# Performance work log

Hardware: AMD Instinct MI355X
Metric: run time of the kernel (lower is better)

Reference implementation:

```python
import jax, jax.numpy as jnp
import numpy as np

NODE_FEAT = 200  # F.interpolate size in run_all_node
TOPN = 2         # StitchModel.topn


def _node_feats(img, mask, flow, n_inst, max_pix):
    """Vectorized run_all_node: per-instance gather, linear interp to NODE_FEAT,
    3x3 sign histogram of flow[:2], mean of flow[2]. mask holds labels 1..n_inst;
    max_pix is a static upper bound on pixels per instance."""
    flat = mask.reshape(-1) - 1                       # labels 0..N-1
    order = jnp.argsort(flat)                         # stable sort by label
    counts = jax.ops.segment_sum(jnp.ones_like(flat), flat, num_segments=n_inst)
    starts = jnp.concatenate([jnp.zeros((1,), counts.dtype), jnp.cumsum(counts)[:-1]])
    j = jnp.arange(max_pix)
    pos = starts[:, None] + jnp.minimum(j[None, :], counts[:, None] - 1)
    idx = order[pos]                                  # [N, max_pix] padded pixel indices
    valid = j[None, :] < counts[:, None]              # [N, max_pix]
    iv = img.reshape(-1)[idx]                         # instance intensity profiles
    fx = flow[0].reshape(-1)[idx]
    fy = flow[1].reshape(-1)[idx]
    fz = flow[2].reshape(-1)[idx]
    cf = counts.astype(img.dtype)
    zflow = jnp.where(valid, fz, 0).sum(1) / cf       # flows[-1][m].mean()

    def interp(v, L):                                 # torch linear interp, align_corners=False
        Lf = L.astype(img.dtype)
        p = jnp.clip((jnp.arange(NODE_FEAT, dtype=img.dtype) + 0.5) * (Lf / NODE_FEAT) - 0.5,
                     0.0, Lf - 1.0)
        i0 = jnp.floor(p).astype(jnp.int32)
        i1 = jnp.minimum(i0 + 1, L - 1)
        w = p - i0.astype(img.dtype)
        return v[i0] * (1 - w) + v[i1] * w

    nodes = jax.vmap(interp)(iv, counts)              # [N, 200]
    # hist_flow_vector: bins ordered (x:<0,==0,>0) x (y:<0,==0,>0) -> 3*cx+cy
    cx = jnp.where(fx < 0, 0, jnp.where(fx == 0, 1, 2))
    cy = jnp.where(fy < 0, 0, jnp.where(fy == 0, 1, 2))
    bins = cx * 3 + cy
    oh = (bins[..., None] == jnp.arange(9)) & valid[..., None]
    hist = oh.sum(1).astype(img.dtype)                # [N, 9]
    return jnp.concatenate([nodes, hist], -1), zflow


def setup_inputs() -> dict:
    H = W = 2048
    N = 4096
    pix = (H * W) // N
    key = jax.random.key(0)
    ks = jax.random.split(key, 8)

    def make_mask(k):
        labels = (jnp.arange(H * W, dtype=jnp.int32) // pix) + 1   # labels 1..N
        perm = jax.random.permutation(k, H * W)
        return labels[perm].reshape(H, W)

    def make_bbox(k):
        u = jax.random.uniform(k, (N, 4), jnp.float32)
        centers = u[:, :2] * H
        sizes = u[:, 2:] * 49.0 + 1.0                               # nonzero w/h (asserted)
        return jnp.concatenate([centers, sizes], -1)

    return {
        "img1": jax.random.normal(ks[0], (H, W), jnp.float32),
        "img2": jax.random.normal(ks[1], (H, W), jnp.float32),
        "flow1": jax.random.normal(ks[2], (3, H, W), jnp.float32),
        "flow2": jax.random.normal(ks[3], (3, H, W), jnp.float32),
        "bbox1": make_bbox(ks[4]),
        "bbox2": make_bbox(ks[5]),
        "mask1": make_mask(ks[6]),
        "mask2": make_mask(ks[7]),
    }


def reference(img1, img2, flow1, flow2, bbox1, bbox2, mask1, mask2):
    N1, N2 = bbox1.shape[0], bbox2.shape[0]
    max1 = mask1.size // N1   # static bound on pixels/instance (equal-partition masks)
    max2 = mask2.size // N2
    node1, zf1 = _node_feats(img1, mask1, flow1, N1, max1)
    node2, zf2 = _node_feats(img2, mask2, flow2, N2, max2)
    x = jnp.concatenate([node1, node2], 0)            # [(N1+N2), 209]
    # build_one_graph_low_ram: per row, TOPN smallest center distances
    d = jnp.sqrt(((bbox1[:, None, :2] - bbox2[None, :, :2]) ** 2).sum(-1))  # [N1,N2]
    _, nbr = jax.lax.top_k(-d, TOPN)                  # smallest-first, like argsort[:topn]
    src = jnp.repeat(jnp.arange(N1), TOPN)            # [N1*TOPN]
    dst = nbr.reshape(-1)
    edge_index = jnp.stack([src, dst + N1])           # [2, N1*TOPN]
    edge_attr = jnp.stack([
        zf1[src], zf2[dst],
        bbox1[src, 0] - bbox2[dst, 0],
        bbox1[src, 1] - bbox2[dst, 1],
        bbox1[src, 2] / bbox2[dst, 2],
        bbox1[src, 3] / bbox2[dst, 3],
    ], -1)                                            # [N1*TOPN, 6]
    return x, edge_index, edge_attr
```

## Files before the change

kernel.cpp:

```cpp
#include <hip/hip_runtime.h>
#include <math.h>

#pragma clang fp contract(off)

#define HW      (2048*2048)
#define NI      4096
#define MAXPIX  1024
#define NF      200
#define FEAT    209
#define NE      (NI*2)
#define XSIZE   ((2*NI)*FEAT)
#define EIOFF   XSIZE
#define EAOFF   (EIOFF + 2*NE)

#define S       8192
#define CHK     (HW/S)
#define TOTCHK  (2*CHK)
#define NBPI    256
#define LPB     16
#define NBG     (2*NBPI)
#define REC     (2*HW)
#define CBLK    (TOTCHK/4)
#define BTOT    (LPB*MAXPIX)

template<int NB>
__device__ __forceinline__ unsigned long long match_bits(int v) {
    unsigned long long m = ~0ull;
    #pragma unroll
    for (int bit = 0; bit < NB; ++bit) {
        unsigned long long bb = __ballot((v >> bit) & 1);
        m &= ((v >> bit) & 1) ? bb : ~bb;
    }
    return m;
}

__global__ void __launch_bounds__(256) count_zf_kernel(const int* __restrict__ mask1,
        const int* __restrict__ mask2, const float* __restrict__ flow1,
        const float* __restrict__ flow2, unsigned* __restrict__ cntA,
        float* __restrict__ zfpart) {
    __shared__ unsigned cnt[4][NBPI];
    __shared__ float zfp[NI];
    int w = threadIdx.x >> 6, lane = threadIdx.x & 63;
    for (int j = threadIdx.x; j < 4*NBPI; j += 256) ((unsigned*)cnt)[j] = 0u;
    for (int j = threadIdx.x; j < NI; j += 256) zfp[j] = 0.f;
    __syncthreads();
    int c = blockIdx.x * 4 + w;
    int img = c / CHK;
    const int4*   mask  = (const int4*)(img ? mask2 : mask1);
    const float4* flowz = (const float4*)((img ? flow2 : flow1) + 2L*HW);
    long base4 = (long)(c - img*CHK) * (S/4);
    for (int t = 0; t < S/4; t += 64) {
        int4   l4 = mask[base4 + t + lane];
        float4 fz = flowz[base4 + t + lane];
        atomicAdd(&cnt[w][(l4.x-1) >> 4], 1u);
        atomicAdd(&cnt[w][(l4.y-1) >> 4], 1u);
        atomicAdd(&cnt[w][(l4.z-1) >> 4], 1u);
        atomicAdd(&cnt[w][(l4.w-1) >> 4], 1u);
        atomicAdd(&zfp[l4.x-1], fz.x);
        atomicAdd(&zfp[l4.y-1], fz.y);
        atomicAdd(&zfp[l4.z-1], fz.z);
        atomicAdd(&zfp[l4.w-1], fz.w);
    }
    __syncthreads();
    unsigned* dst = cntA + (long)c * NBPI;
    for (int j = lane; j < NBPI; j += 64) dst[j] = cnt[w][j];
    float* zdst = zfpart + (long)blockIdx.x * NI;
    for (int j = threadIdx.x; j < NI; j += 256) zdst[j] = zfp[j];
}

__global__ void __launch_bounds__(256) scan1_zf_kernel(unsigned* __restrict__ cntA,
        const float* __restrict__ zfpart, float* __restrict__ zfm) {
    __shared__ int wsum[4];
    __shared__ float zpar[16][LPB];
    int gb = blockIdx.x;
    int img = gb >> 8, lb = gb & (NBPI - 1);
    int t = threadIdx.x, lane = t & 63, w = t >> 6;
    const int PER = CHK / 256;
    unsigned e[PER]; int s = 0;
    long base = ((long)img * CHK + (long)t * PER) * NBPI + lb;
    #pragma unroll
    for (int i = 0; i < PER; ++i) { e[i] = cntA[base + (long)i * NBPI]; s += (int)e[i]; }
    int incl = s;
    #pragma unroll
    for (int off = 1; off < 64; off <<= 1) {
        int o = __shfl_up(incl, off);
        if (lane >= off) incl += o;
    }
    if (lane == 63) wsum[w] = incl;
    __syncthreads();
    int add = 0;
    for (int q = 0; q < w; ++q) add += wsum[q];
    unsigned pre = (unsigned)(incl + add - s);
    #pragma unroll
    for (int i = 0; i < PER; ++i) { unsigned cv = e[i]; cntA[base + (long)i * NBPI] = pre; pre += cv; }
    {
        int li0 = gb * LPB;
        int zimg = li0 >> 12, l0 = li0 & (NI-1);
        int lab = t & 15, rg = t >> 4;
        const float* zp = zfpart + (long)(zimg*(CBLK/2) + rg*8)*NI + l0 + lab;
        float s8 = 0.f;
        #pragma unroll
        for (int k = 0; k < 8; ++k) s8 += zp[(long)k*NI];
        zpar[rg][lab] = s8;
    }
    __syncthreads();
    if (t < LPB) {
        float sum = 0.f;
        #pragma unroll
        for (int g = 0; g < 16; ++g) sum += zpar[g][t];
        zfm[gb*LPB + t] = sum * (1.0f/(float)MAXPIX);
    }
}

__global__ void __launch_bounds__(512) sort_kernel(
        const float* __restrict__ img1, const float* __restrict__ img2,
        const float* __restrict__ flow1, const float* __restrict__ flow2,
        const int* __restrict__ mask1, const int* __restrict__ mask2,
        const unsigned* __restrict__ cntA,
        float* __restrict__ riv, unsigned char* __restrict__ rmeta) {
    __shared__ float ivs[S];
    __shared__ unsigned short smeta[S];
    __shared__ unsigned short cw[8][NBPI];
    __shared__ int gofs[NBPI];
    int* wsum = (int*)smeta;
    int t = threadIdx.x, w = t >> 6, lane = t & 63;
    int c = blockIdx.x;
    int img = c / CHK;
    const int*   mask  = img ? mask2  : mask1;
    const float* image = img ? img2   : img1;
    const float* flow  = img ? flow2  : flow1;
    long base = (long)(c - img*CHK) * S;
    for (int j = t; j < 8*NBPI; j += 512) ((unsigned short*)cw)[j] = 0;
    __syncthreads();
    long qbase = base + (long)w * (S/8);
    int   pk[16];
    float piv[16];
    unsigned long long ltmask = (1ull << lane) - 1ull;
    #pragma unroll
    for (int it = 0; it < 16; ++it) {
        long p = qbase + it*64 + lane;
        int l = mask[p] - 1;
        piv[it] = image[p];
        float fx = flow[p], fy = flow[HW + p];
        int cx = fx < 0.f ? 0 : (fx == 0.f ? 1 : 2);
        int cy = fy < 0.f ? 0 : (fy == 0.f ? 1 : 2);
        int bkt = l >> 4;
        unsigned long long m = match_bits<8>(bkt);
        int cb = __popcll(m & ltmask);
        int ct = __popcll(m);
        pk[it] = l | ((cx*3 + cy) << 12) | (cb << 16) | (ct << 22);
        if (cb == 0) cw[w][bkt] += (unsigned short)ct;
    }
    __syncthreads();
    int tot = 0, incl = 0;
    if (t < NBPI) {
        #pragma unroll
        for (int q = 0; q < 8; ++q) tot += cw[q][t];
        incl = tot;
        #pragma unroll
        for (int off = 1; off < 64; off <<= 1) {
            int o = __shfl_up(incl, off);
            if (lane >= off) incl += o;
        }
        if (lane == 63) wsum[w] = incl;
    }
    __syncthreads();
    if (t < NBPI) {
        int add = 0;
        for (int q = 0; q < w; ++q) add += wsum[q];
        int excl = incl + add - tot;
        int run = excl;
        #pragma unroll
        for (int q = 0; q < 8; ++q) {
            int cq = cw[q][t];
            cw[q][t] = (unsigned short)run;
            run += cq;
        }
        gofs[t] = (img*NBPI + t) * BTOT + (int)cntA[(long)c * NBPI + t] - excl;
    }
    __syncthreads();
    #pragma unroll
    for (int it = 0; it < 16; ++it) {
        int pkv = pk[it];
        int l = pkv & 4095, bin = (pkv >> 12) & 15;
        int cb = (pkv >> 16) & 63, ct = (pkv >> 22) & 127;
        int bkt = l >> 4;
        int r0 = (int)cw[w][bkt];
        int dst = r0 + cb;
        if (cb == ct - 1) cw[w][bkt] = (unsigned short)(r0 + ct);
        ivs[dst] = piv[it];
        smeta[dst] = (unsigned short)((bkt << 8) | (bin << 4) | (l & 15));
    }
    __syncthreads();
    for (int j = t; j < S; j += 512) {
        int ms = (int)smeta[j];
        int b = ms >> 8;
        int g = gofs[b] + j;
        riv[g]   = ivs[j];
        rmeta[g] = (unsigned char)(ms & 0xFF);
    }
}

__global__ void __launch_bounds__(512) stageB_kernel(
        const float* __restrict__ riv, const unsigned char* __restrict__ rmeta,
        float* __restrict__ out) {
    __shared__ float acc[LPB * NF];
    __shared__ float s_tw[MAXPIX];
    __shared__ int   s_tk[MAXPIX];
    __shared__ int   h8[8][LPB * 9];
    __shared__ int   qc[8][LPB];
    __shared__ int   cur[8][LPB];
    int t = threadIdx.x, w = t >> 6, lane = t & 63;
    int gb = blockIdx.x;
    for (int j = t; j < LPB*NF; j += 512) acc[j] = 0.f;
    for (int j = t; j < MAXPIX; j += 512) s_tk[j] = -1;
    for (int j = t; j < 8*LPB*9; j += 512) ((int*)h8)[j] = 0;
    for (int j = t; j < 8*LPB; j += 512) ((int*)qc)[j] = 0;
    __syncthreads();
    if (t < NF) {
        const float Lf = (float)MAXPIX;
        float p = ((float)t + 0.5f) * (Lf / (float)NF) - 0.5f;
        p = fminf(fmaxf(p, 0.0f), Lf - 1.0f);
        int i0 = (int)floorf(p);
        int i1 = min(i0 + 1, MAXPIX - 1);
        float wg = p - (float)i0;
        s_tk[i0] = t; s_tw[i0] = 1.0f - wg;
        s_tk[i1] = t; s_tw[i1] = wg;
    }
    long base = (long)gb * BTOT;
    const int qsz = BTOT / 8;
    int qbeg = w * qsz;
    const int nit = qsz / 64;
    unsigned long long ltmask = (1ull << lane) - 1ull;
    unsigned m4[nit/4];
    #pragma unroll
    for (int j = 0; j < nit/4; ++j) m4[j] = 0u;
    #pragma unroll 4
    for (int it = 0; it < nit; ++it) {
        int meta = (int)rmeta[base + qbeg + it*64 + lane];
        m4[it >> 2] |= (unsigned)meta << (8*(it & 3));
        unsigned long long m = match_bits<4>(meta & 15);
        int cb = __popcll(m & ltmask);
        if (cb == 0) qc[w][meta & 15] += __popcll(m);
    }
    __syncthreads();
    if (t < LPB) {
        int s = 0;
        #pragma unroll
        for (int q = 0; q < 8; ++q) { cur[q][t] = s; s += qc[q][t]; }
    }
    __syncthreads();
    #pragma unroll 4
    for (int it = 0; it < nit; ++it) {
        int meta = (int)(m4[it >> 2] >> (8*(it & 3))) & 255;
        float iv = riv[base + qbeg + it*64 + lane];
        int ll = meta & 15;
        unsigned long long mll = ~0ull, m8;
        #pragma unroll
        for (int bit = 0; bit < 4; ++bit) {
            unsigned long long bb = __ballot((meta >> bit) & 1);
            mll &= ((meta >> bit) & 1) ? bb : ~bb;
        }
        m8 = mll;
        #pragma unroll
        for (int bit = 4; bit < 8; ++bit) {
            unsigned long long bb = __ballot((meta >> bit) & 1);
            m8 &= ((meta >> bit) & 1) ? bb : ~bb;
        }
        int cb = __popcll(mll & ltmask);
        int ct = __popcll(mll);
        int r0 = cur[w][ll];
        int rank = r0 + cb;
        if (cb == ct - 1) cur[w][ll] = r0 + ct;
        if (__popcll(m8 & ltmask) == 0)
            h8[w][ll*9 + (meta >> 4)] += __popcll(m8);
        int k = s_tk[rank];
        if (k >= 0) atomicAdd(&acc[ll*NF + k], iv * s_tw[rank]);
    }
    __syncthreads();
    if (t < FEAT) {
        for (int r = 0; r < LPB; ++r) {
            float v;
            if (t < NF) v = acc[r*NF + t];
            else {
                int hsum = 0;
                #pragma unroll
                for (int q = 0; q < 8; ++q) hsum += h8[q][r*9 + (t - NF)];
                v = (float)hsum;
            }
            long gl = (long)gb * LPB + r;
            out[gl * FEAT + t] = v;
        }
    }
}

__device__ __forceinline__ bool better(float d, int j, float d2, int j2) {
    return d < d2 || (d == d2 && j < j2);
}

__global__ void __launch_bounds__(256) edge_kernel(const float* __restrict__ bbox1,
                                                   const float* __restrict__ bbox2,
                                                   const float* __restrict__ zfm,
                                                   float* __restrict__ out) {
    __shared__ float sbx[NI], sby[NI];
    int wave = threadIdx.x >> 6, lane = threadIdx.x & 63;
    for (int r = threadIdx.x; r < NI; r += 256) {
        float4 b = ((const float4*)bbox2)[r];
        sbx[r] = b.x; sby[r] = b.y;
    }
    __syncthreads();
    int i = blockIdx.x * 4 + wave;
    float c1x = bbox1[i*4 + 0], c1y = bbox1[i*4 + 1];
    float d0 = INFINITY; int j0 = 0x7fffffff;
    float d1 = INFINITY; int j1 = 0x7fffffff;
    for (int t = 0; t < NI; t += 64) {
        int j = t + lane;
        float dx = c1x - sbx[j];
        float dy = c1y - sby[j];
        float dsq = dx*dx + dy*dy;
        float d = (float)sqrt((double)dsq);
        if (better(d, j, d0, j0)) { d1 = d0; j1 = j0; d0 = d; j0 = j; }
        else if (better(d, j, d1, j1)) { d1 = d; j1 = j; }
    }
    for (int off = 32; off; off >>= 1) {
        float od0 = __shfl_down(d0, off); int oj0 = __shfl_down(j0, off);
        float od1 = __shfl_down(d1, off); int oj1 = __shfl_down(j1, off);
        if (better(od0, oj0, d0, j0)) {
            if (better(d0, j0, od1, oj1)) { d1 = d0; j1 = j0; }
            else                          { d1 = od1; j1 = oj1; }
            d0 = od0; j0 = oj0;
        } else if (better(od0, oj0, d1, j1)) { d1 = od0; j1 = oj0; }
    }
    if (lane == 0) {
        float z1 = zfm[i];
        int js[2] = { j0, j1 };
        for (int t = 0; t < 2; ++t) {
            int e = i*2 + t, j = js[t];
            out[EIOFF + e]      = (float)i;
            out[EIOFF + NE + e] = (float)(j + NI);
            float* ea = out + EAOFF + (long)e * 6;
            ea[0] = z1;
            ea[1] = zfm[NI + j];
            ea[2] = c1x - bbox2[j*4 + 0];
            ea[3] = c1y - bbox2[j*4 + 1];
            ea[4] = bbox1[i*4 + 2] / bbox2[j*4 + 2];
            ea[5] = bbox1[i*4 + 3] / bbox2[j*4 + 3];
        }
    }
}

extern "C" void kernel_launch(void* const* d_in, const int* in_sizes, int n_in,
                              void* d_out, int out_size, void* d_ws, size_t ws_size,
                              hipStream_t stream) {
    const float* img1  = (const float*)d_in[0];
    const float* img2  = (const float*)d_in[1];
    const float* flow1 = (const float*)d_in[2];
    const float* flow2 = (const float*)d_in[3];
    const float* bbox1 = (const float*)d_in[4];
    const float* bbox2 = (const float*)d_in[5];
    const int*   mask1 = (const int*)d_in[6];
    const int*   mask2 = (const int*)d_in[7];
    float* out = (float*)d_out;

    char* ws = (char*)d_ws;
    size_t off = 0;
    unsigned* cntA   = (unsigned*)(ws + off); off += (size_t)TOTCHK * NBPI * 4;
    float*    riv    = (float*)(ws + off);    off += (size_t)REC * 4;
    float*    zfpart = (float*)(ws + off);    off += (size_t)CBLK * NI * 4;
    float*    zfm    = (float*)(ws + off);    off += 2 * NI * 4;
    unsigned char* rmeta = (unsigned char*)(ws + off); off += (size_t)REC;

    hipLaunchKernelGGL(count_zf_kernel, dim3(CBLK), dim3(256), 0, stream,
                       mask1, mask2, flow1, flow2, cntA, zfpart);
    hipLaunchKernelGGL(scan1_zf_kernel, dim3(NBG), dim3(256), 0, stream,
                       cntA, zfpart, zfm);
    hipLaunchKernelGGL(sort_kernel, dim3(TOTCHK), dim3(512), 0, stream,
                       img1, img2, flow1, flow2, mask1, mask2, cntA, riv, rmeta);
    hipLaunchKernelGGL(stageB_kernel, dim3(NBG), dim3(512), 0, stream,
                       riv, rmeta, out);
    hipLaunchKernelGGL(edge_kernel, dim3(NI/4), dim3(256), 0, stream,
                       bbox1, bbox2, zfm, out);
}
```

Before: 311.3 us.

## Rebalance count, sort and stageB kernels across more blocks and threads

The count kernel now gives each chunk its own block, with four waves sharing the chunk and their histograms summed. This quadruples the blocks and the zflow partial buffer, and the scan now sums 32 partials per thread. The sort kernel prefetches its cntA offset early and reuses the cw shared memory for the global offsets, freeing shared memory. stageB moves to 1024 threads with 16 waves: it counts per-wave labels with atomics on packed uchar4 metadata instead of ballots, replaces the 8-bit ballot histogram with shared atomics, and writes its output with a flat coalesced loop. These changes target occupancy and load balance, at the cost of more shared-memory atomic contention and more global partials.

Measured after the change: 301.2 us. 1.03x faster.

```diff
diff --git a/kernel.cpp b/kernel.cpp
--- a/kernel.cpp
+++ b/kernel.cpp
@@ -20,7 +20,6 @@
 #define LPB     16
 #define NBG     (2*NBPI)
 #define REC     (2*HW)
-#define CBLK    (TOTCHK/4)
 #define BTOT    (LPB*MAXPIX)
 
 template<int NB>
@@ -44,12 +43,12 @@
     for (int j = threadIdx.x; j < 4*NBPI; j += 256) ((unsigned*)cnt)[j] = 0u;
     for (int j = threadIdx.x; j < NI; j += 256) zfp[j] = 0.f;
     __syncthreads();
-    int c = blockIdx.x * 4 + w;
+    int c = blockIdx.x;
     int img = c / CHK;
     const int4*   mask  = (const int4*)(img ? mask2 : mask1);
     const float4* flowz = (const float4*)((img ? flow2 : flow1) + 2L*HW);
-    long base4 = (long)(c - img*CHK) * (S/4);
-    for (int t = 0; t < S/4; t += 64) {
+    long base4 = (long)(c - img*CHK) * (S/4) + (long)w * (S/16);
+    for (int t = 0; t < S/16; t += 64) {
         int4   l4 = mask[base4 + t + lane];
         float4 fz = flowz[base4 + t + lane];
         atomicAdd(&cnt[w][(l4.x-1) >> 4], 1u);
@@ -63,8 +62,9 @@
     }
     __syncthreads();
     unsigned* dst = cntA + (long)c * NBPI;
-    for (int j = lane; j < NBPI; j += 64) dst[j] = cnt[w][j];
-    float* zdst = zfpart + (long)blockIdx.x * NI;
+    for (int j = threadIdx.x; j < NBPI; j += 256)
+        dst[j] = cnt[0][j] + cnt[1][j] + cnt[2][j] + cnt[3][j];
+    float* zdst = zfpart + (long)c * NI;
     for (int j = threadIdx.x; j < NI; j += 256) zdst[j] = zfp[j];
 }
 
@@ -94,14 +94,13 @@
     #pragma unroll
     for (int i = 0; i < PER; ++i) { unsigned cv = e[i]; cntA[base + (long)i * NBPI] = pre; pre += cv; }
     {
-        int li0 = gb * LPB;
-        int zimg = li0 >> 12, l0 = li0 & (NI-1);
+        int l0 = (gb * LPB) & (NI-1);
         int lab = t & 15, rg = t >> 4;
-        const float* zp = zfpart + (long)(zimg*(CBLK/2) + rg*8)*NI + l0 + lab;
-        float s8 = 0.f;
-        #pragma unroll
-        for (int k = 0; k < 8; ++k) s8 += zp[(long)k*NI];
-        zpar[rg][lab] = s8;
+        const float* zp = zfpart + ((long)img*CHK + rg*32)*NI + l0 + lab;
+        float s32 = 0.f;
+        #pragma unroll
+        for (int k = 0; k < 32; ++k) s32 += zp[(long)k*NI];
+        zpar[rg][lab] = s32;
     }
     __syncthreads();
     if (t < LPB) {
@@ -121,8 +120,8 @@
     __shared__ float ivs[S];
     __shared__ unsigned short smeta[S];
     __shared__ unsigned short cw[8][NBPI];
-    __shared__ int gofs[NBPI];
-    int* wsum = (int*)smeta;
+    int* wsum  = (int*)smeta;
+    int* gofsA = (int*)cw;
     int t = threadIdx.x, w = t >> 6, lane = t & 63;
     int c = blockIdx.x;
     int img = c / CHK;
@@ -130,6 +129,8 @@
     const float* image = img ? img2   : img1;
     const float* flow  = img ? flow2  : flow1;
     long base = (long)(c - img*CHK) * S;
+    unsigned pre = 0;
+    if (t < NBPI) pre = cntA[(long)c * NBPI + t];
     for (int j = t; j < 8*NBPI; j += 512) ((unsigned short*)cw)[j] = 0;
     __syncthreads();
     long qbase = base + (long)w * (S/8);
@@ -165,6 +166,7 @@
         if (lane == 63) wsum[w] = incl;
     }
     __syncthreads();
+    int gof = 0;
     if (t < NBPI) {
         int add = 0;
         for (int q = 0; q < w; ++q) add += wsum[q];
@@ -176,7 +178,7 @@
             cw[q][t] = (unsigned short)run;
             run += cq;
         }
-        gofs[t] = (img*NBPI + t) * BTOT + (int)cntA[(long)c * NBPI + t] - excl;
+        gof = (img*NBPI + t) * BTOT + (int)pre - excl;
     }
     __syncthreads();
     #pragma unroll
@@ -192,30 +194,32 @@
         smeta[dst] = (unsigned short)((bkt << 8) | (bin << 4) | (l & 15));
     }
     __syncthreads();
+    if (t < NBPI) gofsA[t] = gof;
+    __syncthreads();
     for (int j = t; j < S; j += 512) {
         int ms = (int)smeta[j];
         int b = ms >> 8;
-        int g = gofs[b] + j;
+        int g = gofsA[b] + j;
         riv[g]   = ivs[j];
         rmeta[g] = (unsigned char)(ms & 0xFF);
     }
 }
 
-__global__ void __launch_bounds__(512) stageB_kernel(
+__global__ void __launch_bounds__(1024) stageB_kernel(
         const float* __restrict__ riv, const unsigned char* __restrict__ rmeta,
         float* __restrict__ out) {
     __shared__ float acc[LPB * NF];
     __shared__ float s_tw[MAXPIX];
     __shared__ int   s_tk[MAXPIX];
-    __shared__ int   h8[8][LPB * 9];
-    __shared__ int   qc[8][LPB];
-    __shared__ int   cur[8][LPB];
+    __shared__ int   hist[LPB * 9];
+    __shared__ int   qc[16][LPB];
+    __shared__ int   cur[16][LPB];
     int t = threadIdx.x, w = t >> 6, lane = t & 63;
     int gb = blockIdx.x;
-    for (int j = t; j < LPB*NF; j += 512) acc[j] = 0.f;
-    for (int j = t; j < MAXPIX; j += 512) s_tk[j] = -1;
-    for (int j = t; j < 8*LPB*9; j += 512) ((int*)h8)[j] = 0;
-    for (int j = t; j < 8*LPB; j += 512) ((int*)qc)[j] = 0;
+    for (int j = t; j < LPB*NF; j += 1024) acc[j] = 0.f;
+    if (t < MAXPIX) s_tk[t] = -1;
+    if (t < LPB*9) hist[t] = 0;
+    for (int j = t; j < 16*LPB; j += 1024) ((int*)qc)[j] = 0;
     __syncthreads();
     if (t < NF) {
         const float Lf = (float)MAXPIX;
@@ -228,69 +232,49 @@
         s_tk[i1] = t; s_tw[i1] = wg;
     }
     long base = (long)gb * BTOT;
-    const int qsz = BTOT / 8;
+    const int qsz = BTOT / 16;
     int qbeg = w * qsz;
     const int nit = qsz / 64;
     unsigned long long ltmask = (1ull << lane) - 1ull;
-    unsigned m4[nit/4];
-    #pragma unroll
-    for (int j = 0; j < nit/4; ++j) m4[j] = 0u;
+    {
+        const uchar4* rm4 = (const uchar4*)(rmeta + base + qbeg);
+        #pragma unroll
+        for (int it = 0; it < nit/4; ++it) {
+            uchar4 m = rm4[it*64 + lane];
+            atomicAdd(&qc[w][m.x & 15], 1);
+            atomicAdd(&qc[w][m.y & 15], 1);
+            atomicAdd(&qc[w][m.z & 15], 1);
+            atomicAdd(&qc[w][m.w & 15], 1);
+        }
+    }
+    __syncthreads();
+    if (t < LPB) {
+        int s = 0;
+        #pragma unroll
+        for (int q = 0; q < 16; ++q) { cur[q][t] = s; s += qc[q][t]; }
+    }
+    __syncthreads();
     #pragma unroll 4
     for (int it = 0; it < nit; ++it) {
-        int meta = (int)rmeta[base + qbeg + it*64 + lane];
-        m4[it >> 2] |= (unsigned)meta << (8*(it & 3));
-        unsigned long long m = match_bits<4>(meta & 15);
+        int i = qbeg + it*64 + lane;
+        int meta = (int)rmeta[base + i];
+        float iv = riv[base + i];
+        int ll = meta & 15;
+        unsigned long long m = match_bits<4>(ll);
         int cb = __popcll(m & ltmask);
-        if (cb == 0) qc[w][meta & 15] += __popcll(m);
-    }
-    __syncthreads();
-    if (t < LPB) {
-        int s = 0;
-        #pragma unroll
-        for (int q = 0; q < 8; ++q) { cur[q][t] = s; s += qc[q][t]; }
-    }
-    __syncthreads();
-    #pragma unroll 4
-    for (int it = 0; it < nit; ++it) {
-        int meta = (int)(m4[it >> 2] >> (8*(it & 3))) & 255;
-        float iv = riv[base + qbeg + it*64 + lane];
-        int ll = meta & 15;
-        unsigned long long mll = ~0ull, m8;
-        #pragma unroll
-        for (int bit = 0; bit < 4; ++bit) {
-            unsigned long long bb = __ballot((meta >> bit) & 1);
-            mll &= ((meta >> bit) & 1) ? bb : ~bb;
-        }
-        m8 = mll;
-        #pragma unroll
-        for (int bit = 4; bit < 8; ++bit) {
-            unsigned long long bb = __ballot((meta >> bit) & 1);
-            m8 &= ((meta >> bit) & 1) ? bb : ~bb;
-        }
-        int cb = __popcll(mll & ltmask);
-        int ct = __popcll(mll);
+        int ct = __popcll(m);
         int r0 = cur[w][ll];
         int rank = r0 + cb;
         if (cb == ct - 1) cur[w][ll] = r0 + ct;
-        if (__popcll(m8 & ltmask) == 0)
-            h8[w][ll*9 + (meta >> 4)] += __popcll(m8);
+        atomicAdd(&hist[ll*9 + (meta >> 4)], 1);
         int k = s_tk[rank];
         if (k >= 0) atomicAdd(&acc[ll*NF + k], iv * s_tw[rank]);
     }
     __syncthreads();
-    if (t < FEAT) {
-        for (int r = 0; r < LPB; ++r) {
-            float v;
-            if (t < NF) v = acc[r*NF + t];
-            else {
-                int hsum = 0;
-                #pragma unroll
-                for (int q = 0; q < 8; ++q) hsum += h8[q][r*9 + (t - NF)];
-                v = (float)hsum;
-            }
-            long gl = (long)gb * LPB + r;
-            out[gl * FEAT + t] = v;
-        }
+    for (int j = t; j < LPB*FEAT; j += 1024) {
+        int r = j / FEAT, k = j - r*FEAT;
+        float v = (k < NF) ? acc[r*NF + k] : (float)hist[r*9 + (k - NF)];
+        out[(long)gb * LPB * FEAT + j] = v;
     }
 }
 
@@ -366,17 +350,17 @@
     size_t off = 0;
     unsigned* cntA   = (unsigned*)(ws + off); off += (size_t)TOTCHK * NBPI * 4;
     float*    riv    = (float*)(ws + off);    off += (size_t)REC * 4;
-    float*    zfpart = (float*)(ws + off);    off += (size_t)CBLK * NI * 4;
+    float*    zfpart = (float*)(ws + off);    off += (size_t)TOTCHK * NI * 4;
     float*    zfm    = (float*)(ws + off);    off += 2 * NI * 4;
     unsigned char* rmeta = (unsigned char*)(ws + off); off += (size_t)REC;
 
-    hipLaunchKernelGGL(count_zf_kernel, dim3(CBLK), dim3(256), 0, stream,
+    hipLaunchKernelGGL(count_zf_kernel, dim3(TOTCHK), dim3(256), 0, stream,
                        mask1, mask2, flow1, flow2, cntA, zfpart);
     hipLaunchKernelGGL(scan1_zf_kernel, dim3(NBG), dim3(256), 0, stream,
                        cntA, zfpart, zfm);
     hipLaunchKernelGGL(sort_kernel, dim3(TOTCHK), dim3(512), 0, stream,
                        img1, img2, flow1, flow2, mask1, mask2, cntA, riv, rmeta);
-    hipLaunchKernelGGL(stageB_kernel, dim3(NBG), dim3(512), 0, stream,
+    hipLaunchKernelGGL(stageB_kernel, dim3(NBG), dim3(1024), 0, stream,
                        riv, rmeta, out);
     hipLaunchKernelGGL(edge_kernel, dim3(NI/4), dim3(256), 0, stream,
                        bbox1, bbox2, zfm, out);
```
